# Performance work log

Measured on AMD Instinct MI355X. Metric: run time of the kernel, lower is better.

Reference implementation:

```python
import jax, jax.numpy as jnp
import numpy as np

B = 2048        # batch of observations (vmapped agent)
OBS_DIM = 4096
N_GVFS = 4096
INPUTS_PER_GVF = 16
HID_PER_GVF = 8
N_ACTIONS = 18
TOTAL_FEAT = OBS_DIM + HID_PER_GVF * N_GVFS  # 36864


def setup_inputs() -> dict:
    key = jax.random.key(0)
    k_obs, k_gvf, k_q, k_idx = jax.random.split(key, 4)
    observation = jax.random.normal(k_obs, (B, OBS_DIM), dtype=jnp.float32)
    # per-GVF shared hidden layer weights (no bias): (n_gvfs, hidden, inputs)
    gvf_W = jax.random.normal(k_gvf, (N_GVFS, HID_PER_GVF, INPUTS_PER_GVF), dtype=jnp.float32) * 0.05
    # bias-free Q head over concatenated features: (n_actions, total_feat)
    q_W = jax.random.normal(k_q, (N_ACTIONS, TOTAL_FEAT), dtype=jnp.float32) * 0.02
    gvf_input_idxs = jax.random.randint(k_idx, (N_GVFS, INPUTS_PER_GVF), 0, OBS_DIM)
    return {"observation": observation, "gvf_W": gvf_W, "q_W": q_W,
            "gvf_input_idxs": gvf_input_idxs}


def reference(observation, gvf_W, q_W, gvf_input_idxs):
    # get_gvf_inputs: fancy gather per GVF -> (B, n_gvfs, inputs_per_gvf)
    gvf_inputs = observation[:, gvf_input_idxs]
    # compute_shared_representation of each tiny GVF net: relu(W @ x), vmapped
    gvf_feats = jax.nn.relu(jnp.einsum('bgi,ghi->bgh', gvf_inputs, gvf_W))
    # compute_all_features: concat obs with flattened GVF features
    features = jnp.concatenate(
        [observation, gvf_feats.reshape(observation.shape[0], -1)], axis=-1)
    # output_layer.action_values: bias-free linear Q-head
    q_values = jnp.einsum('bf,af->ba', features, q_W)  # (B, n_actions)
    return q_values
```

## Files before the change

### kernel.cpp

```cpp
#include <hip/hip_runtime.h>

#define B_SZ 2048
#define OBS_DIM 4096
#define N_GVFS 4096
#define IPG 16
#define HPG 8
#define N_ACT 18
#define TOTAL_FEAT (OBS_DIM + HPG * N_GVFS)

#define BT 8
#define NTHREADS 512
#define CHUNK 128
#define NCHUNK (N_GVFS / CHUNK)

#define WS_WT 0u
#define WS_Q 1048576u
#define WS_IDX 2228224u
#define WS_NEED 2359296u

typedef unsigned int u32;
typedef unsigned short u16;
typedef __attribute__((ext_vector_type(2))) __fp16 h2;
union U32H2 { u32 u; h2 h; };

__device__ __forceinline__ u32 pk_f16(float a, float b) {
    U32H2 t; t.h = __builtin_amdgcn_cvt_pkrtz(a, b); return t.u;
}

#if __has_builtin(__builtin_amdgcn_fdot2)
__device__ __forceinline__ float fdot2(u32 a, u32 b, float c) {
    U32H2 x, y; x.u = a; y.u = b;
    return __builtin_amdgcn_fdot2(x.h, y.h, c, false);
}
#else
__device__ __forceinline__ float fdot2(u32 a, u32 b, float c) {
    U32H2 x, y; x.u = a; y.u = b;
    return fmaf((float)x.h.x, (float)y.h.x, fmaf((float)x.h.y, (float)y.h.y, c));
}
#endif

#if __has_builtin(__builtin_amdgcn_perm)
__device__ __forceinline__ u32 lo_pair(u32 A, u32 B) { return __builtin_amdgcn_perm(B, A, 0x05040100u); }
__device__ __forceinline__ u32 hi_pair(u32 A, u32 B) { return __builtin_amdgcn_perm(B, A, 0x07060302u); }
#else
__device__ __forceinline__ u32 lo_pair(u32 A, u32 B) { return (A & 0xFFFFu) | (B << 16); }
__device__ __forceinline__ u32 hi_pair(u32 A, u32 B) { return (A >> 16) | (B & 0xFFFF0000u); }
#endif

__device__ __forceinline__ void gll16(const void* g, void* l) {
    __builtin_amdgcn_global_load_lds(
        (const __attribute__((address_space(1))) unsigned int*)g,
        (__attribute__((address_space(3))) unsigned int*)l, 16, 0, 0);
}
__device__ __forceinline__ void gll4(const void* g, void* l) {
    __builtin_amdgcn_global_load_lds(
        (const __attribute__((address_space(1))) unsigned int*)g,
        (__attribute__((address_space(3))) unsigned int*)l, 4, 0, 0);
}

__global__ __launch_bounds__(256)
void pack_all_kernel(const float* __restrict__ W, const float* __restrict__ qW,
                     const int* __restrict__ gidx, unsigned char* __restrict__ ws) {
    const int bid = blockIdx.x, t = threadIdx.x;
    if (bid < 128) {
        const int id = bid * 256 + t;
        const int g = id >> 3, hh = id & 7;
        const float* src = W + (size_t)g * 128 + hh * 16;
        float w[16];
#pragma unroll
        for (int q4 = 0; q4 < 4; ++q4) {
            const float4 f = *(const float4*)(src + q4 * 4);
            w[q4 * 4 + 0] = f.x; w[q4 * 4 + 1] = f.y; w[q4 * 4 + 2] = f.z; w[q4 * 4 + 3] = f.w;
        }
        u32* dst = (u32*)(ws + WS_WT);
#pragma unroll
        for (int pp = 0; pp < 8; ++pp) {
            const int pe = pp * 2 + (hh >> 2);
            dst[(size_t)(pe * 4096 + g) * 4 + (hh & 3)] = pk_f16(w[2 * pp], w[2 * pp + 1]);
        }
    } else if (bid < 416) {
        const int id = (bid - 128) * 256 + t;
        const int a = id >> 12, g = id & 4095;
        const float* src = qW + (size_t)a * TOTAL_FEAT + OBS_DIM + (size_t)g * 8;
        const float4 f0 = *(const float4*)(src);
        const float4 f1 = *(const float4*)(src + 4);
        u32* dst = (u32*)(ws + WS_Q) + (size_t)(a * 4096 + g) * 4;
        dst[0] = pk_f16(f0.x, f0.y); dst[1] = pk_f16(f0.z, f0.w);
        dst[2] = pk_f16(f1.x, f1.y); dst[3] = pk_f16(f1.z, f1.w);
    } else {
        const int id = (bid - 416) * 256 + t;
        const int i = id >> 12, g = id & 4095;
        const u32 j = (u32)gidx[g * 16 + i];
        ((u16*)(ws + WS_IDX))[(size_t)i * 4096 + g] = (u16)((j << 4) | ((j >> 3) & 3));
    }
}

__global__ __launch_bounds__(NTHREADS)
void fused_kernel(const float* __restrict__ obs,
                  const float* __restrict__ qW,
                  const unsigned char* __restrict__ ws,
                  float* __restrict__ out)
{
    __shared__ __align__(16) unsigned char lds[65536 + 32768 + 36864 + 4096 + 1152];
    unsigned char* const obs_c = lds;
    unsigned char* const wt_c  = lds + 65536;
    unsigned char* const q_c   = lds + 98304;
    unsigned char* const idx_c = lds + 135168;
    float* const red2          = (float*)(lds + 139264);

    const int tid  = threadIdx.x;
    const int b0   = blockIdx.x * BT;
    const int lane = tid & 63;
    const int wv   = tid >> 6;
    const int h    = tid >> 7;
    const int s    = tid & (CHUNK - 1);

    for (int m = 0; m < 32; ++m) {
        const int id = tid + NTHREADS * m;
        const int j = id & 4095, p = id >> 12;
        const float a = obs[(size_t)(b0 + 2 * p) * OBS_DIM + j];
        const float b = obs[(size_t)(b0 + 2 * p + 1) * OBS_DIM + j];
        const int w = p ^ ((j >> 3) & 3);
        *(u32*)(obs_c + j * 16 + w * 4) = pk_f16(a, b);
    }

    float qacc[2][N_ACT];
#pragma unroll
    for (int r = 0; r < 2; ++r)
#pragma unroll
        for (int a = 0; a < N_ACT; ++a) qacc[r][a] = 0.f;

    const unsigned char* wsWt  = ws + WS_WT;
    const unsigned char* wsQ   = ws + WS_Q;
    const unsigned char* wsIdx = ws + WS_IDX;

#pragma unroll 1
    for (int k = 0; k < NCHUNK; ++k) {
        __syncthreads();

        for (int p = wv; p < 50; p += 8) {
            if (p < 16) {
                const unsigned char* src = wsWt + ((size_t)p * 4096 + k * CHUNK) * 16;
                unsigned char* dst = wt_c + p * 2048;
                gll16(src + lane * 16, dst);
                gll16(src + 1024 + lane * 16, dst + 1024);
            } else if (p < 34) {
                const int a = p - 16;
                const unsigned char* src = wsQ + ((size_t)a * 4096 + k * CHUNK) * 16;
                unsigned char* dst = q_c + a * 2048;
                gll16(src + lane * 16, dst);
                gll16(src + 1024 + lane * 16, dst + 1024);
            } else {
                const int i = p - 34;
                const unsigned char* src = wsIdx + ((size_t)i * 4096 + k * CHUNK) * 2;
                gll4(src + lane * 4, idx_c + i * 256);
            }
        }
        __syncthreads();

        int ga[IPG];
#pragma unroll
        for (int i = 0; i < IPG; ++i) {
            const u32 t16 = *(const u16*)(idx_c + i * 256 + s * 2);
            ga[i] = (int)(t16 & 0xFFF0u) + ((((u32)h ^ t16) & 3u) << 2);
        }

        float v0[HPG], v1[HPG];
#pragma unroll
        for (int hh = 0; hh < HPG; ++hh) { v0[hh] = 0.f; v1[hh] = 0.f; }

#pragma unroll
        for (int pp = 0; pp < 8; ++pp) {
            const u32 xA = *(const u32*)(obs_c + ga[2 * pp]);
            const u32 xB = *(const u32*)(obs_c + ga[2 * pp + 1]);
            const u32 x0 = lo_pair(xA, xB);
            const u32 x1 = hi_pair(xA, xB);
            const uint4 wA = *(const uint4*)(wt_c + ((pp * 2 + 0) * CHUNK + s) * 16);
            const uint4 wB = *(const uint4*)(wt_c + ((pp * 2 + 1) * CHUNK + s) * 16);
            v0[0] = fdot2(x0, wA.x, v0[0]); v1[0] = fdot2(x1, wA.x, v1[0]);
            v0[1] = fdot2(x0, wA.y, v0[1]); v1[1] = fdot2(x1, wA.y, v1[1]);
            v0[2] = fdot2(x0, wA.z, v0[2]); v1[2] = fdot2(x1, wA.z, v1[2]);
            v0[3] = fdot2(x0, wA.w, v0[3]); v1[3] = fdot2(x1, wA.w, v1[3]);
            v0[4] = fdot2(x0, wB.x, v0[4]); v1[4] = fdot2(x1, wB.x, v1[4]);
            v0[5] = fdot2(x0, wB.y, v0[5]); v1[5] = fdot2(x1, wB.y, v1[5]);
            v0[6] = fdot2(x0, wB.z, v0[6]); v1[6] = fdot2(x1, wB.z, v1[6]);
            v0[7] = fdot2(x0, wB.w, v0[7]); v1[7] = fdot2(x1, wB.w, v1[7]);
        }

        u32 vp0[4], vp1[4];
#pragma unroll
        for (int hp = 0; hp < 4; ++hp) {
            vp0[hp] = pk_f16(fmaxf(v0[2 * hp], 0.f), fmaxf(v0[2 * hp + 1], 0.f));
            vp1[hp] = pk_f16(fmaxf(v1[2 * hp], 0.f), fmaxf(v1[2 * hp + 1], 0.f));
        }

#pragma unroll
        for (int a = 0; a < N_ACT; ++a) {
            const uint4 qp = *(const uint4*)(q_c + (a * CHUNK + s) * 16);
            float a0 = qacc[0][a], a1 = qacc[1][a];
            a0 = fdot2(vp0[0], qp.x, a0); a1 = fdot2(vp1[0], qp.x, a1);
            a0 = fdot2(vp0[1], qp.y, a0); a1 = fdot2(vp1[1], qp.y, a1);
            a0 = fdot2(vp0[2], qp.z, a0); a1 = fdot2(vp1[2], qp.z, a1);
            a0 = fdot2(vp0[3], qp.w, a0); a1 = fdot2(vp1[3], qp.w, a1);
            qacc[0][a] = a0; qacc[1][a] = a1;
        }
    }

#pragma unroll 1
    for (int jj = 0; jj < OBS_DIM / (CHUNK * 4); ++jj) {
        const int j = (jj * CHUNK + s) * 4;
        const float4 o0 = *(const float4*)(obs + (size_t)(b0 + 2 * h) * OBS_DIM + j);
        const float4 o1 = *(const float4*)(obs + (size_t)(b0 + 2 * h + 1) * OBS_DIM + j);
#pragma unroll
        for (int a = 0; a < N_ACT; ++a) {
            const float4 q4 = *(const float4*)(qW + (size_t)a * TOTAL_FEAT + j);
            qacc[0][a] = fmaf(o0.x, q4.x, fmaf(o0.y, q4.y, fmaf(o0.z, q4.z, fmaf(o0.w, q4.w, qacc[0][a]))));
            qacc[1][a] = fmaf(o1.x, q4.x, fmaf(o1.y, q4.y, fmaf(o1.z, q4.z, fmaf(o1.w, q4.w, qacc[1][a]))));
        }
    }

#pragma unroll
    for (int r = 0; r < 2; ++r)
#pragma unroll
        for (int a = 0; a < N_ACT; ++a) {
            float t = qacc[r][a];
#pragma unroll
            for (int m2 = 1; m2 < 64; m2 <<= 1) t += __shfl_xor(t, m2, 64);
            if (lane == 0) red2[(wv * 2 + r) * N_ACT + a] = t;
        }
    __syncthreads();
    if (tid < BT * N_ACT) {
        const int row = tid / N_ACT, a = tid % N_ACT;
        const int w0 = (row >> 1) * 2, r = row & 1;
        out[(size_t)(b0 + row) * N_ACT + a] =
            red2[(w0 * 2 + r) * N_ACT + a] + red2[((w0 + 1) * 2 + r) * N_ACT + a];
    }
}

__global__ __launch_bounds__(256)
void fallback_kernel(const float* __restrict__ obs, const float* __restrict__ W,
                     const float* __restrict__ qW, const int* __restrict__ gidx,
                     float* __restrict__ out)
{
    const int b = blockIdx.x, t = threadIdx.x;
    float acc[N_ACT];
#pragma unroll
    for (int a = 0; a < N_ACT; ++a) acc[a] = 0.f;
    for (int g = t; g < N_GVFS; g += 256) {
        float v[HPG];
#pragma unroll
        for (int hh = 0; hh < HPG; ++hh) v[hh] = 0.f;
        for (int i = 0; i < IPG; ++i) {
            const float x = obs[(size_t)b * OBS_DIM + gidx[g * 16 + i]];
#pragma unroll
            for (int hh = 0; hh < HPG; ++hh)
                v[hh] = fmaf(x, W[g * 128 + hh * 16 + i], v[hh]);
        }
#pragma unroll
        for (int hh = 0; hh < HPG; ++hh) v[hh] = fmaxf(v[hh], 0.f);
#pragma unroll
        for (int a = 0; a < N_ACT; ++a) {
            float t2 = 0.f;
#pragma unroll
            for (int hh = 0; hh < HPG; ++hh)
                t2 = fmaf(v[hh], qW[(size_t)a * TOTAL_FEAT + OBS_DIM + g * 8 + hh], t2);
            acc[a] += t2;
        }
    }
    for (int j = t; j < OBS_DIM; j += 256) {
        const float x = obs[(size_t)b * OBS_DIM + j];
#pragma unroll
        for (int a = 0; a < N_ACT; ++a)
            acc[a] = fmaf(x, qW[(size_t)a * TOTAL_FEAT + j], acc[a]);
    }
    __shared__ float rr[4][N_ACT];
    const int lane = t & 63, w = t >> 6;
#pragma unroll
    for (int a = 0; a < N_ACT; ++a) {
        float x = acc[a];
#pragma unroll
        for (int m = 1; m < 64; m <<= 1) x += __shfl_xor(x, m, 64);
        if (lane == 0) rr[w][a] = x;
    }
    __syncthreads();
    if (t < N_ACT)
        out[(size_t)b * N_ACT + t] = rr[0][t] + rr[1][t] + rr[2][t] + rr[3][t];
}

extern "C" void kernel_launch(void* const* d_in, const int* in_sizes, int n_in,
                              void* d_out, int out_size, void* d_ws, size_t ws_size,
                              hipStream_t stream) {
    const float* obs  = (const float*)d_in[0];
    const float* gvfW = (const float*)d_in[1];
    const float* qW   = (const float*)d_in[2];
    const int*   gidx = (const int*)d_in[3];
    float* out = (float*)d_out;

    if (ws_size >= WS_NEED) {
        unsigned char* ws = (unsigned char*)d_ws;
        pack_all_kernel<<<dim3(672), dim3(256), 0, stream>>>(gvfW, qW, gidx, ws);
        fused_kernel<<<dim3(B_SZ / BT), dim3(NTHREADS), 0, stream>>>(obs, qW, ws, out);
    } else {
        fallback_kernel<<<dim3(B_SZ), dim3(256), 0, stream>>>(obs, gvfW, qW, gidx, out);
    }
}
```

Baseline: 193.4 us.

## Repack GVF index table per-GVF and remap threads so each wave covers all row pairs

The index table is now stored GVF-major within each 128-GVF chunk, so it loads with 16-byte global-to-LDS copies instead of 4-byte ones. Each thread then reads its 16 indices with two 128-bit LDS loads instead of sixteen 16-bit loads. Threads are remapped so each wave handles 16 GVFs across all 4 row pairs rather than 64 GVFs for one pair. This changes the obs LDS gather and bank pattern, and the final reduction becomes 16-lane shuffles plus an 8-way LDS sum.

```diff
diff --git a/kernel.cpp b/kernel.cpp
--- a/kernel.cpp
+++ b/kernel.cpp
@@ -51,11 +51,6 @@
     __builtin_amdgcn_global_load_lds(
         (const __attribute__((address_space(1))) unsigned int*)g,
         (__attribute__((address_space(3))) unsigned int*)l, 16, 0, 0);
-}
-__device__ __forceinline__ void gll4(const void* g, void* l) {
-    __builtin_amdgcn_global_load_lds(
-        (const __attribute__((address_space(1))) unsigned int*)g,
-        (__attribute__((address_space(3))) unsigned int*)l, 4, 0, 0);
 }
 
 __global__ __launch_bounds__(256)
@@ -89,9 +84,10 @@
         dst[2] = pk_f16(f1.x, f1.y); dst[3] = pk_f16(f1.z, f1.w);
     } else {
         const int id = (bid - 416) * 256 + t;
-        const int i = id >> 12, g = id & 4095;
+        const int g = id >> 4, i = id & 15;
         const u32 j = (u32)gidx[g * 16 + i];
-        ((u16*)(ws + WS_IDX))[(size_t)i * 4096 + g] = (u16)((j << 4) | ((j >> 3) & 3));
+        ((u16*)(ws + WS_IDX))[(size_t)(g >> 7) * 2048 + (size_t)(g & 127) * 16 + i] =
+            (u16)((j << 4) | ((j >> 3) & 3));
     }
 }
 
@@ -101,7 +97,7 @@
                   const unsigned char* __restrict__ ws,
                   float* __restrict__ out)
 {
-    __shared__ __align__(16) unsigned char lds[65536 + 32768 + 36864 + 4096 + 1152];
+    __shared__ __align__(16) unsigned char lds[65536 + 32768 + 36864 + 4096 + 4608];
     unsigned char* const obs_c = lds;
     unsigned char* const wt_c  = lds + 65536;
     unsigned char* const q_c   = lds + 98304;
@@ -112,8 +108,8 @@
     const int b0   = blockIdx.x * BT;
     const int lane = tid & 63;
     const int wv   = tid >> 6;
-    const int h    = tid >> 7;
-    const int s    = tid & (CHUNK - 1);
+    const int hp   = lane >> 4;
+    const int s    = wv * 16 + (lane & 15);
 
     for (int m = 0; m < 32; ++m) {
         const int id = tid + NTHREADS * m;
@@ -138,7 +134,7 @@
     for (int k = 0; k < NCHUNK; ++k) {
         __syncthreads();
 
-        for (int p = wv; p < 50; p += 8) {
+        for (int p = wv; p < 38; p += 8) {
             if (p < 16) {
                 const unsigned char* src = wsWt + ((size_t)p * 4096 + k * CHUNK) * 16;
                 unsigned char* dst = wt_c + p * 2048;
@@ -151,18 +147,23 @@
                 gll16(src + lane * 16, dst);
                 gll16(src + 1024 + lane * 16, dst + 1024);
             } else {
-                const int i = p - 34;
-                const unsigned char* src = wsIdx + ((size_t)i * 4096 + k * CHUNK) * 2;
-                gll4(src + lane * 4, idx_c + i * 256);
+                const int pi = p - 34;
+                const unsigned char* src = wsIdx + (size_t)k * 4096 + pi * 1024;
+                gll16(src + lane * 16, idx_c + pi * 1024);
             }
         }
         __syncthreads();
 
+        const uint4 iw0 = *(const uint4*)(idx_c + s * 32);
+        const uint4 iw1 = *(const uint4*)(idx_c + s * 32 + 16);
+        const u32 iw[8] = {iw0.x, iw0.y, iw0.z, iw0.w, iw1.x, iw1.y, iw1.z, iw1.w};
         int ga[IPG];
 #pragma unroll
-        for (int i = 0; i < IPG; ++i) {
-            const u32 t16 = *(const u16*)(idx_c + i * 256 + s * 2);
-            ga[i] = (int)(t16 & 0xFFF0u) + ((((u32)h ^ t16) & 3u) << 2);
+        for (int q2 = 0; q2 < 8; ++q2) {
+            const u32 lo = iw[q2] & 0xFFFFu;
+            const u32 hi = iw[q2] >> 16;
+            ga[2 * q2 + 0] = (int)(lo & 0xFFF0u) + ((((u32)hp ^ lo) & 3u) << 2);
+            ga[2 * q2 + 1] = (int)(hi & 0xFFF0u) + ((((u32)hp ^ hi) & 3u) << 2);
         }
 
         float v0[HPG], v1[HPG];
@@ -189,9 +190,9 @@
 
         u32 vp0[4], vp1[4];
 #pragma unroll
-        for (int hp = 0; hp < 4; ++hp) {
-            vp0[hp] = pk_f16(fmaxf(v0[2 * hp], 0.f), fmaxf(v0[2 * hp + 1], 0.f));
-            vp1[hp] = pk_f16(fmaxf(v1[2 * hp], 0.f), fmaxf(v1[2 * hp + 1], 0.f));
+        for (int hq = 0; hq < 4; ++hq) {
+            vp0[hq] = pk_f16(fmaxf(v0[2 * hq], 0.f), fmaxf(v0[2 * hq + 1], 0.f));
+            vp1[hq] = pk_f16(fmaxf(v1[2 * hq], 0.f), fmaxf(v1[2 * hq + 1], 0.f));
         }
 
 #pragma unroll
@@ -209,8 +210,8 @@
 #pragma unroll 1
     for (int jj = 0; jj < OBS_DIM / (CHUNK * 4); ++jj) {
         const int j = (jj * CHUNK + s) * 4;
-        const float4 o0 = *(const float4*)(obs + (size_t)(b0 + 2 * h) * OBS_DIM + j);
-        const float4 o1 = *(const float4*)(obs + (size_t)(b0 + 2 * h + 1) * OBS_DIM + j);
+        const float4 o0 = *(const float4*)(obs + (size_t)(b0 + 2 * hp) * OBS_DIM + j);
+        const float4 o1 = *(const float4*)(obs + (size_t)(b0 + 2 * hp + 1) * OBS_DIM + j);
 #pragma unroll
         for (int a = 0; a < N_ACT; ++a) {
             const float4 q4 = *(const float4*)(qW + (size_t)a * TOTAL_FEAT + j);
@@ -224,16 +225,22 @@
 #pragma unroll
         for (int a = 0; a < N_ACT; ++a) {
             float t = qacc[r][a];
-#pragma unroll
-            for (int m2 = 1; m2 < 64; m2 <<= 1) t += __shfl_xor(t, m2, 64);
-            if (lane == 0) red2[(wv * 2 + r) * N_ACT + a] = t;
+            t += __shfl_xor(t, 1, 64);
+            t += __shfl_xor(t, 2, 64);
+            t += __shfl_xor(t, 4, 64);
+            t += __shfl_xor(t, 8, 64);
+            if ((lane & 15) == 0)
+                red2[((wv * 4 + hp) * 2 + r) * N_ACT + a] = t;
         }
     __syncthreads();
     if (tid < BT * N_ACT) {
         const int row = tid / N_ACT, a = tid % N_ACT;
-        const int w0 = (row >> 1) * 2, r = row & 1;
-        out[(size_t)(b0 + row) * N_ACT + a] =
-            red2[(w0 * 2 + r) * N_ACT + a] + red2[((w0 + 1) * 2 + r) * N_ACT + a];
+        const int hg = row >> 1, r = row & 1;
+        float sum = 0.f;
+#pragma unroll
+        for (int w2 = 0; w2 < 8; ++w2)
+            sum += red2[((w2 * 4 + hg) * 2 + r) * N_ACT + a];
+        out[(size_t)(b0 + row) * N_ACT + a] = sum;
     }
 }
 
```

After: 184.8 us. -4.4%, faster.
